# Kernel optimization log

Hardware: AMD Instinct MI355X
Metric: run time of the kernel (lower is better)

The kernel has to match this reference:

```python
import jax, jax.numpy as jnp
import numpy as np

SLOPE = 0.1
EPS = 1e-5


def setup_inputs() -> dict:
    key = jax.random.key(0)
    ks = jax.random.split(key, 12)
    C, INTER, RED = 256, 128, 32
    B, H, W = 8, 128, 128
    s = 0.05
    return {
        "x": jax.random.normal(ks[0], (B, C, H, W), jnp.float32),
        "se_w1": jax.random.normal(ks[1], (RED, C), jnp.float32) * s,
        "se_w2": jax.random.normal(ks[2], (C, RED), jnp.float32) * s,
        "wq": jax.random.normal(ks[3], (INTER, C), jnp.float32) * s,
        "bq": jax.random.normal(ks[4], (INTER,), jnp.float32) * s,
        "wk": jax.random.normal(ks[5], (INTER, C), jnp.float32) * s,
        "bk": jax.random.normal(ks[6], (INTER,), jnp.float32) * s,
        "wv": jax.random.normal(ks[7], (INTER, C), jnp.float32) * s,
        "bv": jax.random.normal(ks[8], (INTER,), jnp.float32) * s,
        "w_wg": jax.random.normal(ks[9], (INTER, INTER), jnp.float32) * s,
        "g_wg": jnp.ones((INTER,), jnp.float32),
        "be_wg": jnp.zeros((INTER,), jnp.float32),
        "rm_wg": jnp.zeros((INTER,), jnp.float32),
        "rv_wg": jnp.ones((INTER,), jnp.float32),
        "w_out": jax.random.normal(ks[10], (C, INTER), jnp.float32) * s,
        "b_out": jax.random.normal(ks[11], (C,), jnp.float32) * s,
        "g_out": jnp.ones((C,), jnp.float32),
        "be_out": jnp.zeros((C,), jnp.float32),
        "rm_out": jnp.zeros((C,), jnp.float32),
        "rv_out": jnp.ones((C,), jnp.float32),
    }


def _bn(x, g, b, rm, rv):
    # eval-mode batch norm over channel axis 1; x: [b, c, ...]
    shape = (1, -1) + (1,) * (x.ndim - 2)
    inv = g / jnp.sqrt(rv + EPS)
    return x * inv.reshape(shape) + (b - rm * inv).reshape(shape)


def reference(x, se_w1, se_w2, wq, bq, wk, bk, wv, bv,
              w_wg, g_wg, be_wg, rm_wg, rv_wg,
              w_out, b_out, g_out, be_out, rm_out, rv_out):
    B, C, H, W = x.shape
    # ---- Speactral_Attention (SE block) ----
    y = x.mean(axis=(2, 3))                                  # [b, c]
    y = jax.nn.leaky_relu(y @ se_w1.T, SLOPE)                # [b, c//8]
    y = jax.nn.sigmoid(y @ se_w2.T)                          # [b, c]
    xs = x * y[:, :, None, None]
    # ---- Spatial_GR ----
    xf = xs.reshape(B, C, H * W)                             # [b, c, n]
    q = jnp.einsum('ic,bcn->bin', wq, xf) + bq[None, :, None]
    k = jnp.einsum('ic,bcn->bin', wk, xf) + bk[None, :, None]
    v = jnp.einsum('ic,bcn->bin', wv, xf) + bv[None, :, None]
    # AV = softmax(q @ v^T) over last dim: [b, i, i]
    att = jax.nn.softmax(jnp.einsum('bin,bjn->bij', q, v), axis=2)
    # bmm(k^T, att) then transpose -> av[b,i,n] = sum_j att[b,j,i] * k[b,j,n]
    av = jnp.einsum('bji,bjn->bin', att, k)                  # [b, inter, n]
    avw = jnp.einsum('oi,bin->bon', w_wg, av)                # conv1d k=1, no bias
    avw = _bn(avw, g_wg, be_wg, rm_wg, rv_wg)
    out = jnp.einsum('co,bon->bcn', w_out, avw) + b_out[None, :, None]
    out = _bn(out.reshape(B, C, H, W), g_out, be_out, rm_out, rv_out)
    return jax.nn.leaky_relu(out + xs, SLOPE)
```

## Files before the change

### kernel.cpp

```cpp
#include <hip/hip_runtime.h>
#include <hip/hip_fp16.h>

#define NPIX 16384
#define CCH 256
#define INTR 128
#define REDD 32
#define NB 8
#define SLOPE 0.1f
#define BNEPS 1e-5f

typedef _Float16 f16x8 __attribute__((ext_vector_type(8)));
typedef __attribute__((ext_vector_type(16))) float f32x16;

#define OFF_GX    0
#define OFF_YM    524288
#define OFF_SC    526336
#define OFF_RS    528384
#define OFF_QS    530432
#define OFF_VS    531456
#define OFF_SWG   532480
#define OFF_TWG   532608
#define OFF_SOUT  532736
#define OFF_TOUT  532992
#define OFF_M     795392
#define OFF_WAV   926464
#define OFF_W2    1188608
#define OFF_W7    1450752
#define OFF_B6    1975040
#define OFF_PART  OFF_M

__device__ __forceinline__ unsigned short h1(float f) {
    __half h = __float2half(f);
    return __half_as_ushort(h);
}

__device__ __forceinline__ uint4 cvt8h(const float4 a, const float4 c) {
    __half2 p0 = __floats2half2_rn(a.x, a.y);
    __half2 p1 = __floats2half2_rn(a.z, a.w);
    __half2 p2 = __floats2half2_rn(c.x, c.y);
    __half2 p3 = __floats2half2_rn(c.z, c.w);
    uint4 r;
    r.x = *(unsigned int*)&p0; r.y = *(unsigned int*)&p1;
    r.z = *(unsigned int*)&p2; r.w = *(unsigned int*)&p3;
    return r;
}

__global__ __launch_bounds__(256) void se_kernel(const float* __restrict__ ymsum,
                                                 const float* __restrict__ se_w1,
                                                 const float* __restrict__ se_w2,
                                                 float* __restrict__ scale,
                                                 float* __restrict__ rsum) {
    int b = blockIdx.x, t = threadIdx.x;
    __shared__ float ys[CCH];
    __shared__ float y1s[REDD];
    float ymr = ymsum[b * CCH + t];
    ys[t] = ymr * (1.f / 16384.f);
    __syncthreads();
    if (t < REDD) {
        float a = 0.f;
        #pragma unroll 4
        for (int c = 0; c < CCH; ++c) a += se_w1[t * CCH + c] * ys[c];
        y1s[t] = a > 0.f ? a : SLOPE * a;
    }
    __syncthreads();
    float a = 0.f;
    #pragma unroll
    for (int r = 0; r < REDD; ++r) a += se_w2[t * REDD + r] * y1s[r];
    float sg = 1.f / (1.f + expf(-a));
    scale[b * CCH + t] = sg;
    rsum[b * CCH + t] = sg * ymr;
}

__global__ __launch_bounds__(256) void prep_kernel(const float* __restrict__ g_wg, const float* __restrict__ be_wg,
                                                   const float* __restrict__ rm_wg, const float* __restrict__ rv_wg,
                                                   const float* __restrict__ g_out, const float* __restrict__ be_out,
                                                   const float* __restrict__ rm_out, const float* __restrict__ rv_out,
                                                   float* __restrict__ swg, float* __restrict__ twg,
                                                   float* __restrict__ sout, float* __restrict__ tout) {
    int t = threadIdx.x;
    if (t < INTR) {
        float s = g_wg[t] / sqrtf(rv_wg[t] + BNEPS);
        swg[t] = s;
        twg[t] = be_wg[t] - rm_wg[t] * s;
    }
    float s = g_out[t] / sqrtf(rv_out[t] + BNEPS);
    sout[t] = s;
    tout[t] = be_out[t] - rm_out[t] * s;
}

__global__ __launch_bounds__(256) void qsvs_kernel(const float* __restrict__ wq,
                                                   const float* __restrict__ wv,
                                                   const float* __restrict__ rsum,
                                                   float* __restrict__ qs, float* __restrict__ vs) {
    int b = blockIdx.x, t = threadIdx.x;
    __shared__ float rs[CCH];
    rs[t] = rsum[b * CCH + t];
    __syncthreads();
    const float* w = (t < INTR) ? (wq + t * CCH) : (wv + (t - INTR) * CCH);
    float a = 0.f;
    #pragma unroll 4
    for (int c = 0; c < CCH; ++c) a += w[c] * rs[c];
    if (t < INTR) qs[b * INTR + t] = a;
    else          vs[b * INTR + (t - INTR)] = a;
}

__global__ __launch_bounds__(256, 4) void gram_partial_kernel(const float* __restrict__ x,
                                                              float* __restrict__ partials,
                                                              float* __restrict__ ymsum,
                                                              int nch) {
    __shared__ __align__(16) unsigned short Ah[128 * 64];
    __shared__ __align__(16) unsigned short Bh[128 * 64];
    int bid = blockIdx.x;
    int chunk = bid % nch;
    int t2 = bid / nch;
    int tile = t2 % 3;
    int b = t2 / 3;
    int rowbase = (tile == 1) ? 128 : 0;
    int colbase = (tile == 0) ? 0 : 128;
    bool diag = (tile < 2);
    const float* xb = x + (size_t)b * CCH * NPIX;
    int kpb = NPIX / nch;
    int n0 = chunk * kpb;
    int nsteps = kpb >> 6;
    int tid = threadIdx.x;
    int l = tid & 63, w = tid >> 6;
    int wrow = (w >> 1) * 64, wcol = (w & 1) * 64;

    f32x16 acc[2][2];
    #pragma unroll
    for (int i = 0; i < 2; ++i)
        #pragma unroll
        for (int j = 0; j < 2; ++j)
            #pragma unroll
            for (int r = 0; r < 16; ++r) acc[i][j][r] = 0.f;
    float rowacc[4] = {0.f, 0.f, 0.f, 0.f};

    for (int step = 0; step < nsteps; ++step) {
        int k0 = n0 + step * 64;
        __syncthreads();
        #pragma unroll
        for (int e = 0; e < 4; ++e) {
            int slot = tid + 256 * e;
            int r = slot >> 3, sg = slot & 7;
            const float* src = &xb[(size_t)(rowbase + r) * NPIX + k0 + sg * 8];
            float4 v0 = *(const float4*)src;
            float4 v1 = *(const float4*)(src + 4);
            if (diag) rowacc[e] += (v0.x + v0.y) + (v0.z + v0.w) + (v1.x + v1.y) + (v1.z + v1.w);
            int dst = r * 64 + ((sg ^ (r & 7)) << 3);
            *(uint4*)&Ah[dst] = cvt8h(v0, v1);
            if (!diag) {
                const float* src2 = &xb[(size_t)(colbase + r) * NPIX + k0 + sg * 8];
                float4 u0 = *(const float4*)src2;
                float4 u1 = *(const float4*)(src2 + 4);
                *(uint4*)&Bh[dst] = cvt8h(u0, u1);
            }
        }
        __syncthreads();
        const unsigned short* BP = diag ? Ah : Bh;
        #pragma unroll
        for (int kk = 0; kk < 4; ++kk) {
            int useg = kk * 2 + (l >> 5);
            f16x8 af[2], bf[2];
            #pragma unroll
            for (int at = 0; at < 2; ++at) {
                int r = wrow + at * 32 + (l & 31);
                af[at] = *(const f16x8*)&Ah[r * 64 + ((useg ^ (r & 7)) << 3)];
            }
            #pragma unroll
            for (int bt = 0; bt < 2; ++bt) {
                int c = wcol + bt * 32 + (l & 31);
                bf[bt] = *(const f16x8*)&BP[c * 64 + ((useg ^ (c & 7)) << 3)];
            }
            #pragma unroll
            for (int at = 0; at < 2; ++at)
                #pragma unroll
                for (int bt = 0; bt < 2; ++bt)
                    acc[at][bt] = __builtin_amdgcn_mfma_f32_32x32x16_f16(af[at], bf[bt], acc[at][bt], 0, 0, 0);
        }
    }
    float* P = partials + (size_t)bid * (128 * 128);
    #pragma unroll
    for (int at = 0; at < 2; ++at)
        #pragma unroll
        for (int bt = 0; bt < 2; ++bt)
            #pragma unroll
            for (int r = 0; r < 16; ++r) {
                int lr = wrow + at * 32 + (r & 3) + ((r >> 2) << 3) + ((l >> 5) << 2);
                int lc = wcol + bt * 32 + (l & 31);
                P[lr * 128 + lc] = acc[at][bt][r];
            }
    if (diag) {
        #pragma unroll
        for (int e = 0; e < 4; ++e) {
            float s = rowacc[e];
            s += __shfl_xor(s, 1);
            s += __shfl_xor(s, 2);
            s += __shfl_xor(s, 4);
            if ((tid & 7) == 0) {
                int r = (tid + 256 * e) >> 3;
                atomicAdd(&ymsum[b * CCH + rowbase + r], s);
            }
        }
    }
}

__global__ __launch_bounds__(256) void gram_reduce_kernel(const float* __restrict__ partials,
                                                          float* __restrict__ Gx,
                                                          int nch) {
    int bid = blockIdx.x;
    int part = bid & 15;
    int tileIdx = bid >> 4;
    int tile = tileIdx % 3;
    int b = tileIdx / 3;
    int rowbase = (tile == 1) ? 128 : 0;
    int colbase = (tile == 0) ? 0 : 128;
    int locIdx = part * 1024 + threadIdx.x * 4;
    const float* P = partials + (size_t)tileIdx * nch * (128 * 128) + locIdx;
    float4 s = make_float4(0.f, 0.f, 0.f, 0.f);
    for (int ch = 0; ch < nch; ++ch) {
        float4 v = *(const float4*)(P + (size_t)ch * (128 * 128));
        s.x += v.x; s.y += v.y; s.z += v.z; s.w += v.w;
    }
    int lr = locIdx >> 7, lc = locIdx & 127;
    float* G = Gx + (size_t)b * CCH * CCH;
    *(float4*)&G[(rowbase + lr) * CCH + colbase + lc] = s;
    if (tile == 2) {
        G[(colbase + lc + 0) * CCH + rowbase + lr] = s.x;
        G[(colbase + lc + 1) * CCH + rowbase + lr] = s.y;
        G[(colbase + lc + 2) * CCH + rowbase + lr] = s.z;
        G[(colbase + lc + 3) * CCH + rowbase + lr] = s.w;
    }
}

__global__ __launch_bounds__(256) void ts_kernel(const float* __restrict__ wq,
                                                 const float* __restrict__ scale,
                                                 const float* __restrict__ Gx,
                                                 const float* __restrict__ wv,
                                                 const float* __restrict__ bq,
                                                 const float* __restrict__ bv,
                                                 const float* __restrict__ qs,
                                                 const float* __restrict__ vs,
                                                 float* __restrict__ M) {
    int bid = blockIdx.x;
    int i = bid & 127, b = bid >> 7;
    int t = threadIdx.x;
    __shared__ float sw[CCH];
    __shared__ float t1s[CCH];
    __shared__ float part[256];
    __shared__ float redm[2], reds[2];
    sw[t] = wq[i * CCH + t] * scale[b * CCH + t];
    __syncthreads();
    const float* G = Gx + (size_t)b * CCH * CCH;
    float acc = 0.f;
    #pragma unroll 4
    for (int c = 0; c < CCH; ++c) acc += sw[c] * G[c * CCH + t];
    t1s[t] = acc * scale[b * CCH + t];
    __syncthreads();
    int j = t & 127, h = t >> 7;
    const float* wvr = wv + j * CCH + h * 128;
    const float* tp = t1s + h * 128;
    float p = 0.f;
    #pragma unroll 4
    for (int c = 0; c < 128; ++c) p += tp[c] * wvr[c];
    part[t] = p;
    __syncthreads();
    float acc2 = 0.f;
    if (t < 128)
        acc2 = part[t] + part[t + 128]
             + bq[i] * vs[b * INTR + j] + bv[j] * qs[b * INTR + i] + 16384.f * bq[i] * bv[j];
    float m = acc2;
    for (int off = 32; off > 0; off >>= 1) m = fmaxf(m, __shfl_xor(m, off));
    if (t == 0) redm[0] = m;
    if (t == 64) redm[1] = m;
    __syncthreads();
    m = fmaxf(redm[0], redm[1]);
    float e = expf(acc2 - m);
    float s = e;
    for (int off = 32; off > 0; off >>= 1) s += __shfl_xor(s, off);
    if (t == 0) reds[0] = s;
    if (t == 64) reds[1] = s;
    __syncthreads();
    s = reds[0] + reds[1];
    if (t < 128)
        M[(size_t)b * INTR * INTR + j * INTR + i] = e / s;
}

__global__ __launch_bounds__(256) void wav_kernel(const float* __restrict__ M,
                                                  const float* __restrict__ wk,
                                                  float* __restrict__ Wav) {
    int bid = blockIdx.x;
    int i = bid & 127, b = bid >> 7;
    int t = threadIdx.x;
    __shared__ float ms[INTR];
    if (t < INTR) ms[t] = M[(size_t)b * INTR * INTR + i * INTR + t];
    __syncthreads();
    float acc = 0.f;
    #pragma unroll 4
    for (int jj = 0; jj < INTR; ++jj) acc += ms[jj] * wk[jj * CCH + t];
    Wav[(size_t)b * INTR * CCH + i * CCH + t] = acc;
}

__global__ __launch_bounds__(256) void biaschain_kernel(const float* __restrict__ M,
                                                        const float* __restrict__ bk,
                                                        const float* __restrict__ wwg,
                                                        const float* __restrict__ swg,
                                                        const float* __restrict__ twg,
                                                        const float* __restrict__ wout,
                                                        const float* __restrict__ bout,
                                                        const float* __restrict__ sout,
                                                        const float* __restrict__ tout,
                                                        float* __restrict__ b6) {
    int b = blockIdx.x, t = threadIdx.x;
    __shared__ float bavs[INTR], b2s[INTR];
    if (t < INTR) {
        float a = 0.f;
        #pragma unroll 4
        for (int j = 0; j < INTR; ++j) a += M[(size_t)b * INTR * INTR + t * INTR + j] * bk[j];
        bavs[t] = a;
    }
    __syncthreads();
    if (t < INTR) {
        float a = 0.f;
        #pragma unroll 4
        for (int i = 0; i < INTR; ++i) a += wwg[t * INTR + i] * bavs[i];
        b2s[t] = swg[t] * a + twg[t];
    }
    __syncthreads();
    float a = 0.f;
    #pragma unroll 4
    for (int o = 0; o < INTR; ++o) a += wout[t * INTR + o] * b2s[o];
    float b5 = a + bout[t];
    b6[b * CCH + t] = sout[t] * b5 + tout[t];
}

__global__ __launch_bounds__(256) void w2_kernel(const float* __restrict__ wwg,
                                                 const float* __restrict__ Wav,
                                                 const float* __restrict__ swg,
                                                 float* __restrict__ W2) {
    int bid = blockIdx.x;
    int o = bid & 127, b = bid >> 7;
    int t = threadIdx.x;
    __shared__ float wr[INTR];
    if (t < INTR) wr[t] = wwg[o * INTR + t];
    __syncthreads();
    float acc = 0.f;
    #pragma unroll 4
    for (int i = 0; i < INTR; ++i) acc += wr[i] * Wav[(size_t)b * INTR * CCH + i * CCH + t];
    W2[(size_t)b * INTR * CCH + o * CCH + t] = swg[o] * acc;
}

__global__ __launch_bounds__(256) void w7_kernel(const float* __restrict__ wout,
                                                 const float* __restrict__ W2,
                                                 const float* __restrict__ sout,
                                                 const float* __restrict__ scale,
                                                 unsigned short* __restrict__ W7h) {
    int bid = blockIdx.x;
    int c = bid & 255, b = bid >> 8;
    int t = threadIdx.x;
    __shared__ float wr[INTR];
    if (t < INTR) wr[t] = wout[c * INTR + t];
    __syncthreads();
    float acc = 0.f;
    #pragma unroll 4
    for (int o = 0; o < INTR; ++o) acc += wr[o] * W2[(size_t)b * INTR * CCH + o * CCH + t];
    float w6 = sout[c] * acc + ((c == t) ? 1.f : 0.f);
    W7h[(size_t)b * CCH * CCH + c * CCH + t] = h1(w6 * scale[b * CCH + t]);
}

__global__ __launch_bounds__(256, 4) void final_mfma_kernel(const unsigned short* __restrict__ W7h,
                                                            const float* __restrict__ x,
                                                            const float* __restrict__ b6,
                                                            float* __restrict__ out) {
    __shared__ __align__(16) unsigned short Ws[128 * 64];
    __shared__ __align__(16) unsigned short Xs[128 * 64];
    int bid = blockIdx.x;
    int ct = bid & 1;
    int nt = (bid >> 1) & 127;
    int b = bid >> 8;
    int cbase = ct * 128, n0 = nt * 128;
    const float* xb = x + (size_t)b * CCH * NPIX;
    const unsigned short* Wb = W7h + (size_t)b * CCH * CCH;
    int tid = threadIdx.x;
    int l = tid & 63, w = tid >> 6;
    int wrow = (w >> 1) * 64, wcol = (w & 1) * 64;
    int mn = tid & 31, mk0 = tid >> 5;

    f32x16 acc[2][2];
    #pragma unroll
    for (int i = 0; i < 2; ++i)
        #pragma unroll
        for (int j = 0; j < 2; ++j)
            #pragma unroll
            for (int r = 0; r < 16; ++r) acc[i][j][r] = 0.f;

    for (int step = 0; step < 4; ++step) {
        int k0 = step * 64;
        __syncthreads();
        #pragma unroll
        for (int e = 0; e < 4; ++e) {
            int slot = tid + 256 * e;
            int r = slot >> 3, sg = slot & 7;
            uint4 v = *(const uint4*)&Wb[(size_t)(cbase + r) * CCH + k0 + sg * 8];
            *(uint4*)&Ws[r * 64 + ((sg ^ (r & 7)) << 3)] = v;
        }
        #pragma unroll
        for (int mi = 0; mi < 2; ++mi) {
            int mk = mk0 + mi * 8;
            const float* sp = &xb[(size_t)(k0 + mk * 4) * NPIX + n0 + mn * 4];
            float4 q0 = *(const float4*)sp;
            float4 q1 = *(const float4*)(sp + NPIX);
            float4 q2 = *(const float4*)(sp + 2 * NPIX);
            float4 q3 = *(const float4*)(sp + 3 * NPIX);
            int klo = mk * 4;
            int unit = klo >> 3, sub = (klo & 7) >> 2;
            #pragma unroll
            for (int j = 0; j < 4; ++j) {
                float e0 = j == 0 ? q0.x : j == 1 ? q0.y : j == 2 ? q0.z : q0.w;
                float e1 = j == 0 ? q1.x : j == 1 ? q1.y : j == 2 ? q1.z : q1.w;
                float e2 = j == 0 ? q2.x : j == 1 ? q2.y : j == 2 ? q2.z : q2.w;
                float e3 = j == 0 ? q3.x : j == 1 ? q3.y : j == 2 ? q3.z : q3.w;
                int nl = mn * 4 + j;
                ushort4 cv = make_ushort4(h1(e0), h1(e1), h1(e2), h1(e3));
                int idx = nl * 64 + ((unit ^ ((nl >> 2) & 7)) << 3) + sub * 4;
                *(ushort4*)&Xs[idx] = cv;
            }
        }
        __syncthreads();
        #pragma unroll
        for (int kk = 0; kk < 4; ++kk) {
            int useg = kk * 2 + (l >> 5);
            f16x8 af[2], bfr[2];
            #pragma unroll
            for (int at = 0; at < 2; ++at) {
                int c = wrow + at * 32 + (l & 31);
                af[at] = *(const f16x8*)&Ws[c * 64 + ((useg ^ (c & 7)) << 3)];
            }
            #pragma unroll
            for (int bt = 0; bt < 2; ++bt) {
                int n = wcol + bt * 32 + (l & 31);
                bfr[bt] = *(const f16x8*)&Xs[n * 64 + ((useg ^ ((n >> 2) & 7)) << 3)];
            }
            #pragma unroll
            for (int at = 0; at < 2; ++at)
                #pragma unroll
                for (int bt = 0; bt < 2; ++bt)
                    acc[at][bt] = __builtin_amdgcn_mfma_f32_32x32x16_f16(af[at], bfr[bt], acc[at][bt], 0, 0, 0);
        }
    }
    #pragma unroll
    for (int at = 0; at < 2; ++at)
        #pragma unroll
        for (int bt = 0; bt < 2; ++bt)
            #pragma unroll
            for (int r = 0; r < 16; ++r) {
                int c = cbase + wrow + at * 32 + (r & 3) + ((r >> 2) << 3) + ((l >> 5) << 2);
                int n = n0 + wcol + bt * 32 + (l & 31);
                float v = acc[at][bt][r] + b6[b * CCH + c];
                v = v > 0.f ? v : SLOPE * v;
                out[(size_t)b * CCH * NPIX + (size_t)c * NPIX + n] = v;
            }
}

extern "C" void kernel_launch(void* const* d_in, const int* in_sizes, int n_in,
                              void* d_out, int out_size, void* d_ws, size_t ws_size,
                              hipStream_t stream) {
    (void)in_sizes; (void)n_in; (void)out_size;
    const float* x      = (const float*)d_in[0];
    const float* se_w1  = (const float*)d_in[1];
    const float* se_w2  = (const float*)d_in[2];
    const float* wq     = (const float*)d_in[3];
    const float* bq     = (const float*)d_in[4];
    const float* wk     = (const float*)d_in[5];
    const float* bk     = (const float*)d_in[6];
    const float* wv     = (const float*)d_in[7];
    const float* bv     = (const float*)d_in[8];
    const float* w_wg   = (const float*)d_in[9];
    const float* w_out  = (const float*)d_in[14];
    const float* b_out  = (const float*)d_in[15];
    float* out = (float*)d_out;
    float* ws = (float*)d_ws;

    size_t avail = ws_size / sizeof(float);
    int nch = 32;
    while (nch > 1 && (size_t)OFF_PART + (size_t)NB * 3 * nch * 16384 > avail) nch >>= 1;

    hipMemsetAsync(ws + OFF_YM, 0, (size_t)NB * CCH * sizeof(float), stream);
    gram_partial_kernel<<<NB * 3 * nch, 256, 0, stream>>>(x, ws + OFF_PART, ws + OFF_YM, nch);
    gram_reduce_kernel<<<NB * 3 * 16, 256, 0, stream>>>(ws + OFF_PART, ws + OFF_GX, nch);
    se_kernel<<<NB, 256, 0, stream>>>(ws + OFF_YM, se_w1, se_w2, ws + OFF_SC, ws + OFF_RS);
    prep_kernel<<<1, 256, 0, stream>>>((const float*)d_in[10], (const float*)d_in[11],
                                       (const float*)d_in[12], (const float*)d_in[13],
                                       (const float*)d_in[16], (const float*)d_in[17],
                                       (const float*)d_in[18], (const float*)d_in[19],
                                       ws + OFF_SWG, ws + OFF_TWG, ws + OFF_SOUT, ws + OFF_TOUT);
    qsvs_kernel<<<NB, 256, 0, stream>>>(wq, wv, ws + OFF_RS, ws + OFF_QS, ws + OFF_VS);
    ts_kernel<<<NB * INTR, 256, 0, stream>>>(wq, ws + OFF_SC, ws + OFF_GX, wv, bq, bv,
                                             ws + OFF_QS, ws + OFF_VS, ws + OFF_M);
    wav_kernel<<<NB * INTR, 256, 0, stream>>>(ws + OFF_M, wk, ws + OFF_WAV);
    biaschain_kernel<<<NB, 256, 0, stream>>>(ws + OFF_M, bk, w_wg, ws + OFF_SWG, ws + OFF_TWG,
                                             w_out, b_out, ws + OFF_SOUT, ws + OFF_TOUT, ws + OFF_B6);
    w2_kernel<<<NB * INTR, 256, 0, stream>>>(w_wg, ws + OFF_WAV, ws + OFF_SWG, ws + OFF_W2);
    w7_kernel<<<NB * CCH, 256, 0, stream>>>(w_out, ws + OFF_W2, ws + OFF_SOUT, ws + OFF_SC,
                                            (unsigned short*)(ws + OFF_W7));
    final_mfma_kernel<<<NB * 2 * 128, 256, 0, stream>>>((const unsigned short*)(ws + OFF_W7),
                                                        x, ws + OFF_B6, out);
}
```

Before: 247.6 us.

## Pre-convert input to fp16 once and stream it via direct LDS loads

Adds a conversion kernel that writes an fp16 copy of x and computes per-channel sums. The Gram and final GEMM kernels then read the fp16 copy, using global_load_lds to fill shared memory directly, and Gram partials are stored in fp16. The aim is to halve the bytes read by both GEMMs and remove in-kernel conversion and atomics. In exchange it adds an extra pass over x and a block-order swizzle in the final kernel, and fp16 partials lose precision.

```diff
diff --git a/kernel.cpp b/kernel.cpp
--- a/kernel.cpp
+++ b/kernel.cpp
@@ -27,7 +27,8 @@
 #define OFF_W2    1188608
 #define OFF_W7    1450752
 #define OFF_B6    1975040
-#define OFF_PART  OFF_M
+#define OFF_XH    1977088
+#define OFF_PART  18754304
 
 __device__ __forceinline__ unsigned short h1(float f) {
     __half h = __float2half(f);
@@ -43,6 +44,32 @@
     r.x = *(unsigned int*)&p0; r.y = *(unsigned int*)&p1;
     r.z = *(unsigned int*)&p2; r.w = *(unsigned int*)&p3;
     return r;
+}
+
+__device__ __forceinline__ void gload_lds16(const void* g, void* l) {
+    __builtin_amdgcn_global_load_lds((const __attribute__((address_space(1))) void*)g,
+                                     (__attribute__((address_space(3))) void*)l, 16, 0, 0);
+}
+
+__global__ __launch_bounds__(256) void cvtrow_kernel(const float* __restrict__ x,
+                                                     unsigned short* __restrict__ xh,
+                                                     float* __restrict__ ymsum) {
+    int row = blockIdx.x;
+    const float4* p4 = (const float4*)(x + (size_t)row * NPIX);
+    uint4* o4 = (uint4*)(xh + (size_t)row * NPIX);
+    float s = 0.f;
+    for (int i = threadIdx.x; i < NPIX / 8; i += 256) {
+        float4 v0 = p4[2 * i];
+        float4 v1 = p4[2 * i + 1];
+        s += (v0.x + v0.y) + (v0.z + v0.w) + (v1.x + v1.y) + (v1.z + v1.w);
+        o4[i] = cvt8h(v0, v1);
+    }
+    for (int off = 32; off > 0; off >>= 1) s += __shfl_xor(s, off);
+    __shared__ float red[4];
+    if ((threadIdx.x & 63) == 0) red[threadIdx.x >> 6] = s;
+    __syncthreads();
+    if (threadIdx.x == 0)
+        ymsum[row] = red[0] + red[1] + red[2] + red[3];
 }
 
 __global__ __launch_bounds__(256) void se_kernel(const float* __restrict__ ymsum,
@@ -104,10 +131,9 @@
     else          vs[b * INTR + (t - INTR)] = a;
 }
 
-__global__ __launch_bounds__(256, 4) void gram_partial_kernel(const float* __restrict__ x,
-                                                              float* __restrict__ partials,
-                                                              float* __restrict__ ymsum,
-                                                              int nch) {
+__global__ __launch_bounds__(256) void gram_partial_kernel(const unsigned short* __restrict__ xh,
+                                                           unsigned short* __restrict__ partials,
+                                                           int nch) {
     __shared__ __align__(16) unsigned short Ah[128 * 64];
     __shared__ __align__(16) unsigned short Bh[128 * 64];
     int bid = blockIdx.x;
@@ -118,13 +144,14 @@
     int rowbase = (tile == 1) ? 128 : 0;
     int colbase = (tile == 0) ? 0 : 128;
     bool diag = (tile < 2);
-    const float* xb = x + (size_t)b * CCH * NPIX;
+    const unsigned short* xb = xh + (size_t)b * CCH * NPIX;
     int kpb = NPIX / nch;
     int n0 = chunk * kpb;
     int nsteps = kpb >> 6;
     int tid = threadIdx.x;
     int l = tid & 63, w = tid >> 6;
     int wrow = (w >> 1) * 64, wcol = (w & 1) * 64;
+    int sr = l >> 3, ssg = l & 7;
 
     f32x16 acc[2][2];
     #pragma unroll
@@ -133,27 +160,18 @@
         for (int j = 0; j < 2; ++j)
             #pragma unroll
             for (int r = 0; r < 16; ++r) acc[i][j][r] = 0.f;
-    float rowacc[4] = {0.f, 0.f, 0.f, 0.f};
 
     for (int step = 0; step < nsteps; ++step) {
         int k0 = n0 + step * 64;
         __syncthreads();
         #pragma unroll
         for (int e = 0; e < 4; ++e) {
-            int slot = tid + 256 * e;
-            int r = slot >> 3, sg = slot & 7;
-            const float* src = &xb[(size_t)(rowbase + r) * NPIX + k0 + sg * 8];
-            float4 v0 = *(const float4*)src;
-            float4 v1 = *(const float4*)(src + 4);
-            if (diag) rowacc[e] += (v0.x + v0.y) + (v0.z + v0.w) + (v1.x + v1.y) + (v1.z + v1.w);
-            int dst = r * 64 + ((sg ^ (r & 7)) << 3);
-            *(uint4*)&Ah[dst] = cvt8h(v0, v1);
-            if (!diag) {
-                const float* src2 = &xb[(size_t)(colbase + r) * NPIX + k0 + sg * 8];
-                float4 u0 = *(const float4*)src2;
-                float4 u1 = *(const float4*)(src2 + 4);
-                *(uint4*)&Bh[dst] = cvt8h(u0, u1);
-            }
+            int rbase = e * 32 + w * 8;
+            int r = rbase + sr;
+            int seg = ssg ^ (r & 7);
+            gload_lds16(&xb[(size_t)(rowbase + r) * NPIX + k0 + seg * 8], &Ah[rbase * 64]);
+            if (!diag)
+                gload_lds16(&xb[(size_t)(colbase + r) * NPIX + k0 + seg * 8], &Bh[rbase * 64]);
         }
         __syncthreads();
         const unsigned short* BP = diag ? Ah : Bh;
@@ -178,7 +196,7 @@
                     acc[at][bt] = __builtin_amdgcn_mfma_f32_32x32x16_f16(af[at], bf[bt], acc[at][bt], 0, 0, 0);
         }
     }
-    float* P = partials + (size_t)bid * (128 * 128);
+    unsigned short* P = partials + (size_t)bid * (128 * 128);
     #pragma unroll
     for (int at = 0; at < 2; ++at)
         #pragma unroll
@@ -187,24 +205,11 @@
             for (int r = 0; r < 16; ++r) {
                 int lr = wrow + at * 32 + (r & 3) + ((r >> 2) << 3) + ((l >> 5) << 2);
                 int lc = wcol + bt * 32 + (l & 31);
-                P[lr * 128 + lc] = acc[at][bt][r];
-            }
-    if (diag) {
-        #pragma unroll
-        for (int e = 0; e < 4; ++e) {
-            float s = rowacc[e];
-            s += __shfl_xor(s, 1);
-            s += __shfl_xor(s, 2);
-            s += __shfl_xor(s, 4);
-            if ((tid & 7) == 0) {
-                int r = (tid + 256 * e) >> 3;
-                atomicAdd(&ymsum[b * CCH + rowbase + r], s);
-            }
-        }
-    }
-}
-
-__global__ __launch_bounds__(256) void gram_reduce_kernel(const float* __restrict__ partials,
+                P[lr * 128 + lc] = h1(acc[at][bt][r]);
+            }
+}
+
+__global__ __launch_bounds__(256) void gram_reduce_kernel(const unsigned short* __restrict__ partials,
                                                           float* __restrict__ Gx,
                                                           int nch) {
     int bid = blockIdx.x;
@@ -215,11 +220,14 @@
     int rowbase = (tile == 1) ? 128 : 0;
     int colbase = (tile == 0) ? 0 : 128;
     int locIdx = part * 1024 + threadIdx.x * 4;
-    const float* P = partials + (size_t)tileIdx * nch * (128 * 128) + locIdx;
+    const unsigned short* P = partials + (size_t)tileIdx * nch * (128 * 128) + locIdx;
     float4 s = make_float4(0.f, 0.f, 0.f, 0.f);
     for (int ch = 0; ch < nch; ++ch) {
-        float4 v = *(const float4*)(P + (size_t)ch * (128 * 128));
-        s.x += v.x; s.y += v.y; s.z += v.z; s.w += v.w;
+        ushort4 v = *(const ushort4*)(P + (size_t)ch * (128 * 128));
+        s.x += __half2float(__ushort_as_half(v.x));
+        s.y += __half2float(__ushort_as_half(v.y));
+        s.z += __half2float(__ushort_as_half(v.z));
+        s.w += __half2float(__ushort_as_half(v.w));
     }
     int lr = locIdx >> 7, lc = locIdx & 127;
     float* G = Gx + (size_t)b * CCH * CCH;
@@ -368,22 +376,24 @@
 }
 
 __global__ __launch_bounds__(256, 4) void final_mfma_kernel(const unsigned short* __restrict__ W7h,
-                                                            const float* __restrict__ x,
+                                                            const unsigned short* __restrict__ xh,
                                                             const float* __restrict__ b6,
                                                             float* __restrict__ out) {
     __shared__ __align__(16) unsigned short Ws[128 * 64];
     __shared__ __align__(16) unsigned short Xs[128 * 64];
-    int bid = blockIdx.x;
+    int bid0 = blockIdx.x;
+    int bid = (bid0 & 7) * 256 + (bid0 >> 3);
     int ct = bid & 1;
     int nt = (bid >> 1) & 127;
     int b = bid >> 8;
     int cbase = ct * 128, n0 = nt * 128;
-    const float* xb = x + (size_t)b * CCH * NPIX;
+    const unsigned short* xb = xh + (size_t)b * CCH * NPIX;
     const unsigned short* Wb = W7h + (size_t)b * CCH * CCH;
     int tid = threadIdx.x;
     int l = tid & 63, w = tid >> 6;
     int wrow = (w >> 1) * 64, wcol = (w & 1) * 64;
     int mn = tid & 31, mk0 = tid >> 5;
+    int sr = l >> 3, ssg = l & 7;
 
     f32x16 acc[2][2];
     #pragma unroll
@@ -398,29 +408,29 @@
         __syncthreads();
         #pragma unroll
         for (int e = 0; e < 4; ++e) {
-            int slot = tid + 256 * e;
-            int r = slot >> 3, sg = slot & 7;
-            uint4 v = *(const uint4*)&Wb[(size_t)(cbase + r) * CCH + k0 + sg * 8];
-            *(uint4*)&Ws[r * 64 + ((sg ^ (r & 7)) << 3)] = v;
+            int rbase = e * 32 + w * 8;
+            int r = rbase + sr;
+            int seg = ssg ^ (r & 7);
+            gload_lds16(&Wb[(size_t)(cbase + r) * CCH + k0 + seg * 8], &Ws[rbase * 64]);
         }
         #pragma unroll
         for (int mi = 0; mi < 2; ++mi) {
             int mk = mk0 + mi * 8;
-            const float* sp = &xb[(size_t)(k0 + mk * 4) * NPIX + n0 + mn * 4];
-            float4 q0 = *(const float4*)sp;
-            float4 q1 = *(const float4*)(sp + NPIX);
-            float4 q2 = *(const float4*)(sp + 2 * NPIX);
-            float4 q3 = *(const float4*)(sp + 3 * NPIX);
+            const unsigned short* sp = &xb[(size_t)(k0 + mk * 4) * NPIX + n0 + mn * 4];
+            ushort4 q0 = *(const ushort4*)sp;
+            ushort4 q1 = *(const ushort4*)(sp + NPIX);
+            ushort4 q2 = *(const ushort4*)(sp + 2 * NPIX);
+            ushort4 q3 = *(const ushort4*)(sp + 3 * NPIX);
             int klo = mk * 4;
             int unit = klo >> 3, sub = (klo & 7) >> 2;
             #pragma unroll
             for (int j = 0; j < 4; ++j) {
-                float e0 = j == 0 ? q0.x : j == 1 ? q0.y : j == 2 ? q0.z : q0.w;
-                float e1 = j == 0 ? q1.x : j == 1 ? q1.y : j == 2 ? q1.z : q1.w;
-                float e2 = j == 0 ? q2.x : j == 1 ? q2.y : j == 2 ? q2.z : q2.w;
-                float e3 = j == 0 ? q3.x : j == 1 ? q3.y : j == 2 ? q3.z : q3.w;
+                unsigned short e0 = j == 0 ? q0.x : j == 1 ? q0.y : j == 2 ? q0.z : q0.w;
+                unsigned short e1 = j == 0 ? q1.x : j == 1 ? q1.y : j == 2 ? q1.z : q1.w;
+                unsigned short e2 = j == 0 ? q2.x : j == 1 ? q2.y : j == 2 ? q2.z : q2.w;
+                unsigned short e3 = j == 0 ? q3.x : j == 1 ? q3.y : j == 2 ? q3.z : q3.w;
                 int nl = mn * 4 + j;
-                ushort4 cv = make_ushort4(h1(e0), h1(e1), h1(e2), h1(e3));
+                ushort4 cv = make_ushort4(e0, e1, e2, e3);
                 int idx = nl * 64 + ((unit ^ ((nl >> 2) & 7)) << 3) + sub * 4;
                 *(ushort4*)&Xs[idx] = cv;
             }
@@ -479,14 +489,16 @@
     const float* b_out  = (const float*)d_in[15];
     float* out = (float*)d_out;
     float* ws = (float*)d_ws;
+    unsigned short* xh = (unsigned short*)(ws + OFF_XH);
 
     size_t avail = ws_size / sizeof(float);
     int nch = 32;
-    while (nch > 1 && (size_t)OFF_PART + (size_t)NB * 3 * nch * 16384 > avail) nch >>= 1;
-
-    hipMemsetAsync(ws + OFF_YM, 0, (size_t)NB * CCH * sizeof(float), stream);
-    gram_partial_kernel<<<NB * 3 * nch, 256, 0, stream>>>(x, ws + OFF_PART, ws + OFF_YM, nch);
-    gram_reduce_kernel<<<NB * 3 * 16, 256, 0, stream>>>(ws + OFF_PART, ws + OFF_GX, nch);
+    while (nch > 1 && (size_t)OFF_PART + (size_t)NB * 3 * nch * 8192 > avail) nch >>= 1;
+
+    cvtrow_kernel<<<NB * CCH, 256, 0, stream>>>(x, xh, ws + OFF_YM);
+    gram_partial_kernel<<<NB * 3 * nch, 256, 0, stream>>>(xh, (unsigned short*)(ws + OFF_PART), nch);
+    gram_reduce_kernel<<<NB * 3 * 16, 256, 0, stream>>>((const unsigned short*)(ws + OFF_PART),
+                                                        ws + OFF_GX, nch);
     se_kernel<<<NB, 256, 0, stream>>>(ws + OFF_YM, se_w1, se_w2, ws + OFF_SC, ws + OFF_RS);
     prep_kernel<<<1, 256, 0, stream>>>((const float*)d_in[10], (const float*)d_in[11],
                                        (const float*)d_in[12], (const float*)d_in[13],
@@ -503,5 +515,5 @@
     w7_kernel<<<NB * CCH, 256, 0, stream>>>(w_out, ws + OFF_W2, ws + OFF_SOUT, ws + OFF_SC,
                                             (unsigned short*)(ws + OFF_W7));
     final_mfma_kernel<<<NB * 2 * 128, 256, 0, stream>>>((const unsigned short*)(ws + OFF_W7),
-                                                        x, ws + OFF_B6, out);
-}
+                                                        xh, ws + OFF_B6, out);
+}
```

Result: faster. 238.4 us (-3.7%).
